# Kernel tuning notes

Measured on AMD Instinct MI355X. Metric: run time of the kernel, lower is better.

## Reference

```python
import jax, jax.numpy as jnp
import numpy as np

B = 16384
D = 384
K = 256
BETAS = (0.05, 0.25, 0.6)  # per-level commitment costs


def setup_inputs() -> dict:
    key = jax.random.key(0)
    k0, k1, k2, kc0, kc1, kc2 = jax.random.split(key, 6)
    return {
        "l0": jax.random.normal(k0, (B, 4, D), dtype=jnp.float32),
        "l1": jax.random.normal(k1, (B, 16, D), dtype=jnp.float32),
        "l2": jax.random.normal(k2, (B, 16, D), dtype=jnp.float32),
        "cb0": jax.random.normal(kc0, (K, D), dtype=jnp.float32),
        "cb1": jax.random.normal(kc1, (K, D), dtype=jnp.float32),
        "cb2": jax.random.normal(kc2, (K, D), dtype=jnp.float32),
    }


def _vq(x, cb, beta):
    # x: (B, T, D), cb: (K, D) -> d2: (B, T, K)
    d2 = (jnp.sum(x * x, axis=-1, keepdims=True)
          - 2.0 * jnp.einsum('btd,kd->btk', x, cb)
          + jnp.sum(cb * cb, axis=-1))
    idx = jnp.argmin(d2, axis=-1)            # (B, T) nearest codebook entry
    q = cb[idx]                              # (B, T, D) gather
    # EMA-VQ: codebook updated by EMA, loss is commitment term only
    loss = beta * jnp.mean((jax.lax.stop_gradient(q) - x) ** 2)
    q_st = x + jax.lax.stop_gradient(q - x)  # straight-through estimator
    return q_st, loss, idx


def reference(l0, l1, l2, cb0, cb1, cb2):
    q0, loss0, idx0 = _vq(l0, cb0, BETAS[0])
    q1, loss1, idx1 = _vq(l1, cb1, BETAS[1])
    q2, loss2, idx2 = _vq(l2, cb2, BETAS[2])
    total_vq_loss = loss0 + loss1 + loss2
    return (q0, q1, q2, total_vq_loss, idx0, idx1, idx2)
```

## Files before the change

kernel.cpp:

```cpp
#include <hip/hip_runtime.h>

static constexpr int KN  = 256;
static constexpr int DD  = 384;
static constexpr int DD4 = 96;
static constexpr int TM  = 64;
#define FLAG_MARGIN 0.005f

typedef __attribute__((ext_vector_type(8)))  short bf16x8;
typedef __attribute__((ext_vector_type(16))) float f32x16;
typedef __attribute__((ext_vector_type(4)))  short short4v;

__device__ __forceinline__ unsigned short f2bf_rne(float x) {
  unsigned u = __float_as_uint(x);
  return (unsigned short)((u + 0x7fffu + ((u >> 16) & 1u)) >> 16);
}

__device__ __forceinline__ void g2lds16(const void* g, void* l) {
  __builtin_amdgcn_global_load_lds(
      (const __attribute__((address_space(1))) unsigned int*)g,
      (__attribute__((address_space(3))) unsigned int*)l, 16, 0, 0);
}

__device__ __forceinline__ float emu_sq_pairwise384(const float* __restrict__ p) {
  float S[4];
#pragma unroll
  for (int blk = 0; blk < 4; ++blk) {
    const float* b = p + blk * 96;
    float r[8];
#pragma unroll
    for (int l = 0; l < 8; ++l) r[l] = __fmul_rn(b[l], b[l]);
    for (int j = 8; j < 96; j += 8) {
#pragma unroll
      for (int l = 0; l < 8; ++l) r[l] = __fadd_rn(r[l], __fmul_rn(b[j + l], b[j + l]));
    }
    float t1 = __fadd_rn(__fadd_rn(r[0], r[1]), __fadd_rn(r[2], r[3]));
    float t2 = __fadd_rn(__fadd_rn(r[4], r[5]), __fadd_rn(r[6], r[7]));
    S[blk] = __fadd_rn(t1, t2);
  }
  return __fadd_rn(__fadd_rn(S[0], S[1]), __fadd_rn(S[2], S[3]));
}

__device__ __forceinline__ float emu_dot384_np(const float* __restrict__ x,
                                               const float* __restrict__ c) {
  float s[16];
#pragma unroll
  for (int t = 0; t < 16; ++t) s[t] = 0.f;
  for (int j = 0; j < 384; j += 16) {
#pragma unroll
    for (int t = 0; t < 16; ++t)
      s[t] = __fadd_rn(__fmul_rn(x[j + t], c[j + t]), s[t]);
  }
  float w0 = __fadd_rn(__fadd_rn(s[0], s[4]), __fadd_rn(s[8],  s[12]));
  float w1 = __fadd_rn(__fadd_rn(s[1], s[5]), __fadd_rn(s[9],  s[13]));
  float w2 = __fadd_rn(__fadd_rn(s[2], s[6]), __fadd_rn(s[10], s[14]));
  float w3 = __fadd_rn(__fadd_rn(s[3], s[7]), __fadd_rn(s[11], s[15]));
  return __fadd_rn(__fadd_rn(w0, w1), __fadd_rn(w2, w3));
}

__global__ __launch_bounds__(256) void prep_kernel(const float* __restrict__ c0,
                                                   const float* __restrict__ c1,
                                                   const float* __restrict__ c2,
                                                   float* __restrict__ e2,
                                                   double* __restrict__ delta,
                                                   short* __restrict__ fragbase) {
  int bid = blockIdx.x;
  if (bid < 3) {
    const float* cb = (bid == 0) ? c0 : ((bid == 1) ? c1 : c2);
    e2[bid * KN + threadIdx.x] = emu_sq_pairwise384(cb + (size_t)threadIdx.x * DD);
    if (threadIdx.x == 0) delta[bid] = 0.0;
    return;
  }
  int sb = bid - 3;
  int lvl = sb / 48;
  int blk48 = sb - lvl * 48;
  const float* cb = (lvl == 0) ? c0 : ((lvl == 1) ? c1 : c2);
  short* frag = fragbase + (size_t)lvl * 196608;
  int gid = blk48 * 256 + threadIdx.x;
  int e = gid / 48;
  int g = gid - e * 48;
  const float4* s4 = reinterpret_cast<const float4*>(cb) + (size_t)e * 96 + g * 2;
  float4 v0 = s4[0], v1 = s4[1];
  float xs[8] = {v0.x, v0.y, v0.z, v0.w, v1.x, v1.y, v1.z, v1.w};
  short h[8], l[8];
#pragma unroll
  for (int i = 0; i < 8; ++i) {
    h[i] = (short)f2bf_rne(xs[i]);
    float hf = __uint_as_float((unsigned)(unsigned short)h[i] << 16);
    l[i] = (short)f2bf_rne(xs[i] - hf);
  }
  int c = g >> 2, rem = g & 3, ks = rem >> 1, hs = rem & 1;
  int t = e >> 5, lane = (e & 31) + (hs << 5);
  size_t blk = (((size_t)(c * 8 + t) * 2 + ks) * 2);
  short* dh = frag + blk * 512 + lane * 8;
  short* dl = dh + 512;
  *reinterpret_cast<bf16x8*>(dh) = *reinterpret_cast<const bf16x8*>(h);
  *reinterpret_cast<bf16x8*>(dl) = *reinterpret_cast<const bf16x8*>(l);
}

__global__ __launch_bounds__(256) void vq_main(
    const float* __restrict__ X0, const float* __restrict__ X1, const float* __restrict__ X2,
    const float* __restrict__ C0, const float* __restrict__ C1, const float* __restrict__ C2,
    const short* __restrict__ FRAGBASE,
    const float* __restrict__ E2A,
    float* __restrict__ QBASE,
    float* __restrict__ IDXBASE,
    unsigned char* __restrict__ FLAGBASE,
    double* __restrict__ PART,
    int nb0, int nb1)
{
  __shared__ __align__(16) short cb_lds[2][8192];
  __shared__ __align__(16) short x_lds[2048];
  struct Epi {
    float b1[4][TM]; int i1[4][TM]; float b2[4][TM];
    int idx[TM]; float xx[TM];
  };
  Epi* ep = reinterpret_cast<Epi*>(x_lds);

  const int bid = blockIdx.x;
  int lvl, lb;
  if (bid < nb0)            { lvl = 0; lb = bid; }
  else if (bid < nb0 + nb1) { lvl = 1; lb = bid - nb0; }
  else                      { lvl = 2; lb = bid - nb0 - nb1; }
  const float* X  = (lvl == 0) ? X0 : ((lvl == 1) ? X1 : X2);
  const float* CBF32 = (lvl == 0) ? C0 : ((lvl == 1) ? C1 : C2);
  const short* CBFRAG = FRAGBASE + (size_t)lvl * 196608;
  const float* E2 = E2A + lvl * KN;
  const size_t rowbase = (lvl == 0) ? 0 : ((lvl == 1) ? (size_t)nb0 * TM
                                                      : (size_t)(nb0 + nb1) * TM);
  float* Q = QBASE + rowbase * DD;
  float* IDXO = IDXBASE + rowbase;
  unsigned char* FLAG = FLAGBASE + rowbase;
  const size_t row0 = (size_t)lb * TM;

  const int tid  = threadIdx.x;
  const int wid  = tid >> 6, lane = tid & 63;
  const int lr   = lane & 31, hi = lane >> 5;
  const int r_st = tid >> 2, f4 = tid & 3;

  const float4* X4 = reinterpret_cast<const float4*>(X);
  const float4* xsrc = X4 + (row0 + (size_t)r_st) * DD4 + f4;

  f32x16 acc[4];
  {
    f32x16 z;
#pragma unroll
    for (int i = 0; i < 16; ++i) z[i] = 0.f;
#pragma unroll
    for (int i = 0; i < 4; ++i) acc[i] = z;
  }
  float xx = 0.f;

  const int xboff = (r_st >> 5) * 2048;
  const int xpos  = ((f4 >> 1) * 32 + (r_st & 31)) * 16 + (f4 & 1) * 8;

#define STAGE_CB(CN)                                                          \
  {                                                                           \
    int c2_ = (CN) >> 1, ks_ = (CN) & 1;                                      \
    _Pragma("unroll")                                                         \
    for (int s = 0; s < 4; ++s) {                                             \
      int idx = s * 256 + tid;                                                \
      int b = idx >> 6;                                                       \
      const char* src = (const char*)CBFRAG                                   \
          + (((size_t)(c2_ * 8 + (b >> 1)) * 4 + ks_ * 2 + (b & 1)) << 10)    \
          + (idx & 63) * 16;                                                  \
      g2lds16(src, (char*)cb_lds[(CN) & 1] + idx * 16);                       \
    }                                                                         \
  }

#define CVT_WRITE_X(XF)                                                       \
  {                                                                           \
    float a_[4] = {(XF).x, (XF).y, (XF).z, (XF).w};                           \
    short hh_[4], ll_[4];                                                     \
    _Pragma("unroll")                                                         \
    for (int i = 0; i < 4; ++i) {                                             \
      xx = fmaf(a_[i], a_[i], xx);                                            \
      unsigned u_ = __float_as_uint(a_[i]);                                   \
      unsigned t_ = u_ + 0x7fffu + ((u_ >> 16) & 1u);                         \
      hh_[i] = (short)(t_ >> 16);                                             \
      float hf_ = __uint_as_float(t_ & 0xffff0000u);                          \
      float lf_ = a_[i] - hf_;                                                \
      ll_[i] = (short)(__float_as_uint(lf_) >> 16);                           \
    }                                                                         \
    char* xb_ = (char*)x_lds;                                                 \
    *reinterpret_cast<short4v*>(xb_ + xboff + xpos) =                         \
        *reinterpret_cast<short4v*>(hh_);                                     \
    *reinterpret_cast<short4v*>(xb_ + xboff + 1024 + xpos) =                  \
        *reinterpret_cast<short4v*>(ll_);                                     \
  }

  STAGE_CB(0);
  {
    float4 xf0 = xsrc[0];
    CVT_WRITE_X(xf0);
  }
  __syncthreads();

#pragma unroll 1
  for (int c = 0; c < 24; ++c) {
    float4 xfn;
    if (c < 23) {
      STAGE_CB(c + 1);
      xfn = xsrc[(c + 1) * 4];
    }

    const char* xb = (const char*)x_lds;
    bf16x8 ah0 = *reinterpret_cast<const bf16x8*>(xb +        lane * 16);
    bf16x8 al0 = *reinterpret_cast<const bf16x8*>(xb + 1024 + lane * 16);
    bf16x8 ah1 = *reinterpret_cast<const bf16x8*>(xb + 2048 + lane * 16);
    bf16x8 al1 = *reinterpret_cast<const bf16x8*>(xb + 3072 + lane * 16);
    const bf16x8* bb = reinterpret_cast<const bf16x8*>(cb_lds[c & 1]);
#pragma unroll
    for (int cti = 0; cti < 2; ++cti) {
      int t = wid * 2 + cti;
      bf16x8 bh = bb[(t * 2 + 0) * 64 + lane];
      bf16x8 bl = bb[(t * 2 + 1) * 64 + lane];
      acc[cti]     = __builtin_amdgcn_mfma_f32_32x32x16_bf16(ah0, bh, acc[cti], 0, 0, 0);
      acc[cti]     = __builtin_amdgcn_mfma_f32_32x32x16_bf16(ah0, bl, acc[cti], 0, 0, 0);
      acc[cti]     = __builtin_amdgcn_mfma_f32_32x32x16_bf16(al0, bh, acc[cti], 0, 0, 0);
      acc[2 + cti] = __builtin_amdgcn_mfma_f32_32x32x16_bf16(ah1, bh, acc[2 + cti], 0, 0, 0);
      acc[2 + cti] = __builtin_amdgcn_mfma_f32_32x32x16_bf16(ah1, bl, acc[2 + cti], 0, 0, 0);
      acc[2 + cti] = __builtin_amdgcn_mfma_f32_32x32x16_bf16(al1, bh, acc[2 + cti], 0, 0, 0);
    }

    __syncthreads();
    if (c < 23) {
      CVT_WRITE_X(xfn);
      __syncthreads();
    }
  }

  {
    float t = xx;
    t += __shfl_xor(t, 1);
    t += __shfl_xor(t, 2);
    if (f4 == 0) ep->xx[r_st] = t;
  }

  float e2v[2];
  e2v[0] = E2[wid * 64 + lr];
  e2v[1] = E2[wid * 64 + 32 + lr];
  const int c0i = wid * 64 + lr, c1i = wid * 64 + 32 + lr;

#pragma unroll
  for (int rt = 0; rt < 2; ++rt) {
#pragma unroll
    for (int v = 0; v < 16; ++v) {
      int row = rt * 32 + (v & 3) + 8 * (v >> 2) + 4 * hi;
      float s0 = e2v[0] - 2.0f * acc[rt * 2 + 0][v];
      float s1 = e2v[1] - 2.0f * acc[rt * 2 + 1][v];
      float b1; int i1;
      if (s0 <= s1) { b1 = s0; i1 = c0i; } else { b1 = s1; i1 = c1i; }
#pragma unroll
      for (int m = 1; m < 32; m <<= 1) {
        float ob = __shfl_xor(b1, m);
        int   oi = __shfl_xor(i1, m);
        if (ob < b1 || (ob == b1 && oi < i1)) { b1 = ob; i1 = oi; }
      }
      float b2 = 1e30f;
      if (c0i != i1 && s0 < b2) b2 = s0;
      if (c1i != i1 && s1 < b2) b2 = s1;
#pragma unroll
      for (int m = 1; m < 32; m <<= 1) {
        float ob = __shfl_xor(b2, m);
        if (ob < b2) b2 = ob;
      }
      if (lr == 0) {
        ep->b1[wid][row] = b1; ep->i1[wid][row] = i1; ep->b2[wid][row] = b2;
      }
    }
  }
  __syncthreads();

  double lrow = 0.0;
  if (tid < TM) {
    float b1 = ep->b1[0][tid]; int i1 = ep->i1[0][tid]; float b2 = ep->b2[0][tid];
#pragma unroll
    for (int w = 1; w < 4; ++w) {
      float ob1 = ep->b1[w][tid]; int oi1 = ep->i1[w][tid]; float ob2 = ep->b2[w][tid];
      if (ob1 < b1 || (ob1 == b1 && oi1 < i1)) {
        b2 = fminf(b1, ob2); b1 = ob1; i1 = oi1;
      } else {
        b2 = fminf(b2, ob1);
      }
    }
    ep->idx[tid] = i1;
    IDXO[row0 + tid] = (float)i1;
    FLAG[row0 + tid] = (b2 - b1 < FLAG_MARGIN) ? 1 : 0;
    lrow = (double)ep->xx[tid] + (double)b1;
  }
  if (tid < 64) {
#pragma unroll
    for (int m = 1; m < 64; m <<= 1) lrow += __shfl_xor(lrow, m);
    if (tid == 0) PART[bid] = lrow;
  }
  __syncthreads();

  const float4* CB4 = reinterpret_cast<const float4*>(CBF32);
  float4* Q4 = reinterpret_cast<float4*>(Q);
  for (int i = tid; i < TM * DD4; i += 256) {
    int r = i / DD4;
    int cc = i - r * DD4;
    Q4[(row0 + (size_t)r) * DD4 + cc] = CB4[(size_t)ep->idx[r] * DD4 + cc];
  }
}

__global__ __launch_bounds__(256) void vq_refine(
    const float* __restrict__ X0, const float* __restrict__ X1, const float* __restrict__ X2,
    const float* __restrict__ C0, const float* __restrict__ C1, const float* __restrict__ C2,
    const float* __restrict__ E2A,
    const unsigned char* __restrict__ F0, const unsigned char* __restrict__ F1,
    const unsigned char* __restrict__ F2,
    int r0, int r1, int r2,
    float* __restrict__ Q0, float* __restrict__ Q1, float* __restrict__ Q2,
    float* __restrict__ I0, float* __restrict__ I1, float* __restrict__ I2,
    double* __restrict__ DELTA)
{
  const int lane   = threadIdx.x & 63;
  const int gwave  = (blockIdx.x * blockDim.x + threadIdx.x) >> 6;
  const int nwaves = (gridDim.x * blockDim.x) >> 6;
  const int ntot = r0 + r1 + r2;

  for (int base = gwave * 64; base < ntot; base += nwaves * 64) {
    int lvl, lb;
    const float *X, *CB; const unsigned char* FLAG; float *Q, *IDXO;
    if (base < r0)           { lvl = 0; lb = base;            X = X0; CB = C0; FLAG = F0; Q = Q0; IDXO = I0; }
    else if (base < r0 + r1) { lvl = 1; lb = base - r0;       X = X1; CB = C1; FLAG = F1; Q = Q1; IDXO = I1; }
    else                     { lvl = 2; lb = base - r0 - r1;  X = X2; CB = C2; FLAG = F2; Q = Q2; IDXO = I2; }
    const float* E2EMU = E2A + lvl * KN;

    unsigned char f = FLAG[lb + lane];
    unsigned long long mask = __ballot(f != 0);
    while (mask) {
      int bit = __ffsll((long long)mask) - 1;
      mask &= mask - 1;
      const int r = lb + bit;
      const float* xr = X + (size_t)r * DD;
      const float xx = emu_sq_pairwise384(xr);

      float best = 1e30f; int bidx = 0x7fffffff;
#pragma unroll
      for (int t = 0; t < 4; ++t) {
        int k = lane * 4 + t;
        const float* ck = CB + (size_t)k * DD;
        float E = emu_dot384_np(xr, ck);
        float s = __fadd_rn(__fsub_rn(xx, __fmul_rn(2.0f, E)), E2EMU[k]);
        if (s < best || (s == best && k < bidx)) { best = s; bidx = k; }
      }
#pragma unroll
      for (int m = 1; m < 64; m <<= 1) {
        float ob = __shfl_xor(best, m);
        int   oi = __shfl_xor(bidx, m);
        if (ob < best || (ob == best && oi < bidx)) { best = ob; bidx = oi; }
      }

      const int old = (int)IDXO[r];
      if (bidx != old) {
        const float* cn = CB + (size_t)bidx * DD;
        const float* co = CB + (size_t)old * DD;
        double dl = 0.0;
        for (int d = lane; d < DD; d += 64) {
          float xv = xr[d];
          float qn = cn[d], qo = co[d];
          Q[(size_t)r * DD + d] = qn;
          double en = (double)qn - (double)xv;
          double eo = (double)qo - (double)xv;
          dl += en * en - eo * eo;
        }
#pragma unroll
        for (int m = 1; m < 64; m <<= 1) dl += __shfl_xor(dl, m);
        if (lane == 0) {
          atomicAdd(DELTA + lvl, dl);
          IDXO[r] = (float)bidx;
        }
      }
    }
  }
}

__global__ void finalize_kernel(const double* __restrict__ p0, int n0, double w0,
                                const double* __restrict__ p1, int n1, double w1,
                                const double* __restrict__ p2, int n2, double w2,
                                const double* __restrict__ delta,
                                float* __restrict__ out) {
  __shared__ double red[4];
  int tid = threadIdx.x;
  double s0 = 0.0, s1 = 0.0, s2 = 0.0;
  for (int i = tid; i < n0; i += 256) s0 += p0[i];
  for (int i = tid; i < n1; i += 256) s1 += p1[i];
  for (int i = tid; i < n2; i += 256) s2 += p2[i];
  double v = s0 * w0 + s1 * w1 + s2 * w2;
#pragma unroll
  for (int m = 1; m < 64; m <<= 1) v += __shfl_xor(v, m);
  if ((tid & 63) == 0) red[tid >> 6] = v;
  __syncthreads();
  if (tid == 0)
    out[0] = (float)(red[0] + red[1] + red[2] + red[3]
                     + delta[0] * w0 + delta[1] * w1 + delta[2] * w2);
}

extern "C" void kernel_launch(void* const* d_in, const int* in_sizes, int n_in,
                              void* d_out, int out_size, void* d_ws, size_t ws_size,
                              hipStream_t stream) {
  const float* l0  = (const float*)d_in[0];
  const float* l1  = (const float*)d_in[1];
  const float* l2  = (const float*)d_in[2];
  const float* cb0 = (const float*)d_in[3];
  const float* cb1 = (const float*)d_in[4];
  const float* cb2 = (const float*)d_in[5];

  const size_t n_q0 = (size_t)in_sizes[0];
  const size_t n_q1 = (size_t)in_sizes[1];
  const size_t n_q2 = (size_t)in_sizes[2];
  const int r0 = (int)(n_q0 / DD);
  const int r1 = (int)(n_q1 / DD);
  const int r2 = (int)(n_q2 / DD);

  float* out   = (float*)d_out;
  float* q0    = out;
  float* q1    = q0 + n_q0;
  float* q2    = q1 + n_q1;
  float* lossp = q2 + n_q2;
  float* idx0  = lossp + 1;
  float* idx1  = idx0 + r0;
  float* idx2  = idx1 + r1;

  float*  e2    = (float*)d_ws;
  double* part  = (double*)((char*)d_ws + 4096);
  double* delta = (double*)((char*)d_ws + 4096 + 73728);
  unsigned char* flag0 = (unsigned char*)d_ws + 4096 + 73728 + 1024;
  unsigned char* flag1 = flag0 + r0;
  unsigned char* flag2 = flag1 + r1;
  short* cbf0 = (short*)((char*)d_ws + (1 << 20));

  const int nb0 = r0 / TM, nb1 = r1 / TM, nb2 = r2 / TM;
  double* p0 = part;
  double* p1 = p0 + nb0;
  double* p2 = p1 + nb1;

  prep_kernel<<<147, 256, 0, stream>>>(cb0, cb1, cb2, e2, delta, cbf0);

  vq_main<<<nb0 + nb1 + nb2, 256, 0, stream>>>(
      l0, l1, l2, cb0, cb1, cb2, cbf0, e2,
      q0, idx0, flag0, part, nb0, nb1);

  vq_refine<<<512, 256, 0, stream>>>(l0, l1, l2, cb0, cb1, cb2, e2,
                                     flag0, flag1, flag2, r0, r1, r2,
                                     q0, q1, q2, idx0, idx1, idx2, delta);

  const double w0 = 0.05 / ((double)r0 * DD);
  const double w1 = 0.25 / ((double)r1 * DD);
  const double w2 = 0.60 / ((double)r2 * DD);
  finalize_kernel<<<1, 256, 0, stream>>>(p0, nb0, w0, p1, nb1, w1, p2, nb2, w2,
                                         delta, lossp);
}
```

Measured before the change: 883.0 us.

## Use 512-thread blocks in vq_main, one 32-column tile per wave, single-buffered k-chunks

Doubles vq_main's block size to 8 waves so each wave owns 32 codebook columns instead of 64. The K loop now takes 12 steps of 32 elements each, and the double-buffered codebook prefetch overlap is replaced by a single buffer with two barriers per step. The epilogue argmin merge widens to 8 partial results per row. The goal is more parallelism and fewer accumulator registers per wave, at the cost of losing the copy/compute overlap and adding more syncs.

```diff
diff --git a/kernel.cpp b/kernel.cpp
--- a/kernel.cpp
+++ b/kernel.cpp
@@ -97,7 +97,7 @@
   *reinterpret_cast<bf16x8*>(dl) = *reinterpret_cast<const bf16x8*>(l);
 }
 
-__global__ __launch_bounds__(256) void vq_main(
+__global__ __launch_bounds__(512) void vq_main(
     const float* __restrict__ X0, const float* __restrict__ X1, const float* __restrict__ X2,
     const float* __restrict__ C0, const float* __restrict__ C1, const float* __restrict__ C2,
     const short* __restrict__ FRAGBASE,
@@ -108,10 +108,10 @@
     double* __restrict__ PART,
     int nb0, int nb1)
 {
-  __shared__ __align__(16) short cb_lds[2][8192];
-  __shared__ __align__(16) short x_lds[2048];
+  __shared__ __align__(16) short cb_lds[16384];
+  __shared__ __align__(16) short x_lds[4096];
   struct Epi {
-    float b1[4][TM]; int i1[4][TM]; float b2[4][TM];
+    float b1[8][TM]; int i1[8][TM]; float b2[8][TM];
     int idx[TM]; float xx[TM];
   };
   Epi* ep = reinterpret_cast<Epi*>(x_lds);
@@ -135,130 +135,100 @@
   const int tid  = threadIdx.x;
   const int wid  = tid >> 6, lane = tid & 63;
   const int lr   = lane & 31, hi = lane >> 5;
-  const int r_st = tid >> 2, f4 = tid & 3;
+  const int r_st = tid >> 3, k4 = tid & 7;
 
   const float4* X4 = reinterpret_cast<const float4*>(X);
-  const float4* xsrc = X4 + (row0 + (size_t)r_st) * DD4 + f4;
-
-  f32x16 acc[4];
+  const float4* xsrc = X4 + (row0 + (size_t)r_st) * DD4 + k4;
+
+  f32x16 acc[2];
   {
     f32x16 z;
 #pragma unroll
     for (int i = 0; i < 16; ++i) z[i] = 0.f;
-#pragma unroll
-    for (int i = 0; i < 4; ++i) acc[i] = z;
+    acc[0] = z; acc[1] = z;
   }
   float xx = 0.f;
 
-  const int xboff = (r_st >> 5) * 2048;
-  const int xpos  = ((f4 >> 1) * 32 + (r_st & 31)) * 16 + (f4 & 1) * 8;
-
-#define STAGE_CB(CN)                                                          \
-  {                                                                           \
-    int c2_ = (CN) >> 1, ks_ = (CN) & 1;                                      \
-    _Pragma("unroll")                                                         \
-    for (int s = 0; s < 4; ++s) {                                             \
-      int idx = s * 256 + tid;                                                \
-      int b = idx >> 6;                                                       \
-      const char* src = (const char*)CBFRAG                                   \
-          + (((size_t)(c2_ * 8 + (b >> 1)) * 4 + ks_ * 2 + (b & 1)) << 10)    \
-          + (idx & 63) * 16;                                                  \
-      g2lds16(src, (char*)cb_lds[(CN) & 1] + idx * 16);                       \
-    }                                                                         \
-  }
-
-#define CVT_WRITE_X(XF)                                                       \
-  {                                                                           \
-    float a_[4] = {(XF).x, (XF).y, (XF).z, (XF).w};                           \
-    short hh_[4], ll_[4];                                                     \
-    _Pragma("unroll")                                                         \
-    for (int i = 0; i < 4; ++i) {                                             \
-      xx = fmaf(a_[i], a_[i], xx);                                            \
-      unsigned u_ = __float_as_uint(a_[i]);                                   \
-      unsigned t_ = u_ + 0x7fffu + ((u_ >> 16) & 1u);                         \
-      hh_[i] = (short)(t_ >> 16);                                             \
-      float hf_ = __uint_as_float(t_ & 0xffff0000u);                          \
-      float lf_ = a_[i] - hf_;                                                \
-      ll_[i] = (short)(__float_as_uint(lf_) >> 16);                           \
-    }                                                                         \
-    char* xb_ = (char*)x_lds;                                                 \
-    *reinterpret_cast<short4v*>(xb_ + xboff + xpos) =                         \
-        *reinterpret_cast<short4v*>(hh_);                                     \
-    *reinterpret_cast<short4v*>(xb_ + xboff + 1024 + xpos) =                  \
-        *reinterpret_cast<short4v*>(ll_);                                     \
-  }
-
-  STAGE_CB(0);
-  {
-    float4 xf0 = xsrc[0];
-    CVT_WRITE_X(xf0);
-  }
-  __syncthreads();
+  const int xblk = ((r_st >> 5) * 2 + (k4 >> 2)) * 2;
+  const int xpos = (((k4 >> 1) & 1) * 32 + (r_st & 31)) * 16 + (k4 & 1) * 8;
 
 #pragma unroll 1
-  for (int c = 0; c < 24; ++c) {
-    float4 xfn;
-    if (c < 23) {
-      STAGE_CB(c + 1);
-      xfn = xsrc[(c + 1) * 4];
-    }
+  for (int c = 0; c < 12; ++c) {
+#pragma unroll
+    for (int s = 0; s < 4; ++s) {
+      int idx = s * 512 + tid;
+      int b = idx >> 6;
+      const char* src = (const char*)CBFRAG
+          + (((size_t)(c * 8 + (b >> 2)) * 4 + (b & 3)) << 10) + (idx & 63) * 16;
+      g2lds16(src, (char*)cb_lds + idx * 16);
+    }
+    {
+      float4 v = xsrc[c * 8];
+      float a_[4] = {v.x, v.y, v.z, v.w};
+      short hh_[4], ll_[4];
+#pragma unroll
+      for (int i = 0; i < 4; ++i) {
+        xx = fmaf(a_[i], a_[i], xx);
+        unsigned u_ = __float_as_uint(a_[i]);
+        unsigned t_ = u_ + 0x7fffu + ((u_ >> 16) & 1u);
+        hh_[i] = (short)(t_ >> 16);
+        float hf_ = __uint_as_float(t_ & 0xffff0000u);
+        float lf_ = a_[i] - hf_;
+        ll_[i] = (short)(__float_as_uint(lf_) >> 16);
+      }
+      char* xb_ = (char*)x_lds;
+      *reinterpret_cast<short4v*>(xb_ + xblk * 1024 + xpos) =
+          *reinterpret_cast<short4v*>(hh_);
+      *reinterpret_cast<short4v*>(xb_ + (xblk + 1) * 1024 + xpos) =
+          *reinterpret_cast<short4v*>(ll_);
+    }
+    __syncthreads();
 
     const char* xb = (const char*)x_lds;
-    bf16x8 ah0 = *reinterpret_cast<const bf16x8*>(xb +        lane * 16);
-    bf16x8 al0 = *reinterpret_cast<const bf16x8*>(xb + 1024 + lane * 16);
-    bf16x8 ah1 = *reinterpret_cast<const bf16x8*>(xb + 2048 + lane * 16);
-    bf16x8 al1 = *reinterpret_cast<const bf16x8*>(xb + 3072 + lane * 16);
-    const bf16x8* bb = reinterpret_cast<const bf16x8*>(cb_lds[c & 1]);
-#pragma unroll
-    for (int cti = 0; cti < 2; ++cti) {
-      int t = wid * 2 + cti;
-      bf16x8 bh = bb[(t * 2 + 0) * 64 + lane];
-      bf16x8 bl = bb[(t * 2 + 1) * 64 + lane];
-      acc[cti]     = __builtin_amdgcn_mfma_f32_32x32x16_bf16(ah0, bh, acc[cti], 0, 0, 0);
-      acc[cti]     = __builtin_amdgcn_mfma_f32_32x32x16_bf16(ah0, bl, acc[cti], 0, 0, 0);
-      acc[cti]     = __builtin_amdgcn_mfma_f32_32x32x16_bf16(al0, bh, acc[cti], 0, 0, 0);
-      acc[2 + cti] = __builtin_amdgcn_mfma_f32_32x32x16_bf16(ah1, bh, acc[2 + cti], 0, 0, 0);
-      acc[2 + cti] = __builtin_amdgcn_mfma_f32_32x32x16_bf16(ah1, bl, acc[2 + cti], 0, 0, 0);
-      acc[2 + cti] = __builtin_amdgcn_mfma_f32_32x32x16_bf16(al1, bh, acc[2 + cti], 0, 0, 0);
-    }
-
+    const char* bbase = (const char*)cb_lds;
+#pragma unroll
+    for (int ks = 0; ks < 2; ++ks) {
+      bf16x8 ah0 = *reinterpret_cast<const bf16x8*>(xb + ((0 * 2 + ks) * 2 + 0) * 1024 + lane * 16);
+      bf16x8 al0 = *reinterpret_cast<const bf16x8*>(xb + ((0 * 2 + ks) * 2 + 1) * 1024 + lane * 16);
+      bf16x8 ah1 = *reinterpret_cast<const bf16x8*>(xb + ((1 * 2 + ks) * 2 + 0) * 1024 + lane * 16);
+      bf16x8 al1 = *reinterpret_cast<const bf16x8*>(xb + ((1 * 2 + ks) * 2 + 1) * 1024 + lane * 16);
+      bf16x8 bh = *reinterpret_cast<const bf16x8*>(bbase + (wid * 4 + ks * 2 + 0) * 1024 + lane * 16);
+      bf16x8 bl = *reinterpret_cast<const bf16x8*>(bbase + (wid * 4 + ks * 2 + 1) * 1024 + lane * 16);
+      acc[0] = __builtin_amdgcn_mfma_f32_32x32x16_bf16(ah0, bh, acc[0], 0, 0, 0);
+      acc[0] = __builtin_amdgcn_mfma_f32_32x32x16_bf16(ah0, bl, acc[0], 0, 0, 0);
+      acc[0] = __builtin_amdgcn_mfma_f32_32x32x16_bf16(al0, bh, acc[0], 0, 0, 0);
+      acc[1] = __builtin_amdgcn_mfma_f32_32x32x16_bf16(ah1, bh, acc[1], 0, 0, 0);
+      acc[1] = __builtin_amdgcn_mfma_f32_32x32x16_bf16(ah1, bl, acc[1], 0, 0, 0);
+      acc[1] = __builtin_amdgcn_mfma_f32_32x32x16_bf16(al1, bh, acc[1], 0, 0, 0);
+    }
     __syncthreads();
-    if (c < 23) {
-      CVT_WRITE_X(xfn);
-      __syncthreads();
-    }
   }
 
   {
     float t = xx;
     t += __shfl_xor(t, 1);
     t += __shfl_xor(t, 2);
-    if (f4 == 0) ep->xx[r_st] = t;
-  }
-
-  float e2v[2];
-  e2v[0] = E2[wid * 64 + lr];
-  e2v[1] = E2[wid * 64 + 32 + lr];
-  const int c0i = wid * 64 + lr, c1i = wid * 64 + 32 + lr;
+    t += __shfl_xor(t, 4);
+    if ((lane & 7) == 0) ep->xx[r_st] = t;
+  }
+
+  const float e2v = E2[wid * 32 + lr];
+  const int mycol = wid * 32 + lr;
 
 #pragma unroll
   for (int rt = 0; rt < 2; ++rt) {
 #pragma unroll
     for (int v = 0; v < 16; ++v) {
       int row = rt * 32 + (v & 3) + 8 * (v >> 2) + 4 * hi;
-      float s0 = e2v[0] - 2.0f * acc[rt * 2 + 0][v];
-      float s1 = e2v[1] - 2.0f * acc[rt * 2 + 1][v];
-      float b1; int i1;
-      if (s0 <= s1) { b1 = s0; i1 = c0i; } else { b1 = s1; i1 = c1i; }
+      float sc = e2v - 2.0f * acc[rt][v];
+      float b1 = sc; int i1 = mycol;
 #pragma unroll
       for (int m = 1; m < 32; m <<= 1) {
         float ob = __shfl_xor(b1, m);
         int   oi = __shfl_xor(i1, m);
         if (ob < b1 || (ob == b1 && oi < i1)) { b1 = ob; i1 = oi; }
       }
-      float b2 = 1e30f;
-      if (c0i != i1 && s0 < b2) b2 = s0;
-      if (c1i != i1 && s1 < b2) b2 = s1;
+      float b2 = (mycol != i1) ? sc : 1e30f;
 #pragma unroll
       for (int m = 1; m < 32; m <<= 1) {
         float ob = __shfl_xor(b2, m);
@@ -275,7 +245,7 @@
   if (tid < TM) {
     float b1 = ep->b1[0][tid]; int i1 = ep->i1[0][tid]; float b2 = ep->b2[0][tid];
 #pragma unroll
-    for (int w = 1; w < 4; ++w) {
+    for (int w = 1; w < 8; ++w) {
       float ob1 = ep->b1[w][tid]; int oi1 = ep->i1[w][tid]; float ob2 = ep->b2[w][tid];
       if (ob1 < b1 || (ob1 == b1 && oi1 < i1)) {
         b2 = fminf(b1, ob2); b1 = ob1; i1 = oi1;
@@ -297,7 +267,7 @@
 
   const float4* CB4 = reinterpret_cast<const float4*>(CBF32);
   float4* Q4 = reinterpret_cast<float4*>(Q);
-  for (int i = tid; i < TM * DD4; i += 256) {
+  for (int i = tid; i < TM * DD4; i += 512) {
     int r = i / DD4;
     int cc = i - r * DD4;
     Q4[(row0 + (size_t)r) * DD4 + cc] = CB4[(size_t)ep->idx[r] * DD4 + cc];
@@ -439,7 +409,7 @@
 
   prep_kernel<<<147, 256, 0, stream>>>(cb0, cb1, cb2, e2, delta, cbf0);
 
-  vq_main<<<nb0 + nb1 + nb2, 256, 0, stream>>>(
+  vq_main<<<nb0 + nb1 + nb2, 512, 0, stream>>>(
       l0, l1, l2, cb0, cb1, cb2, cbf0, e2,
       q0, idx0, flag0, part, nb0, nb1);
 
```

Result: no change. 898.0 us (+1.7%).
